# Optimization experiments

Measured on AMD Instinct MI355X. Metric: run time of the kernel, lower is better.

## Reference

```python
import jax, jax.numpy as jnp
from jax import lax
import numpy as np

B, C, H, W = 8, 256, 192, 192
ATT_K = 11
BN_EPS = 1e-5


def _dwconv(x, w, pad, stride=1):
    # x: NCHW, w: (C,1,kh,kw) depthwise
    return lax.conv_general_dilated(
        x, w, window_strides=(stride, stride), padding=pad,
        feature_group_count=x.shape[1],
        dimension_numbers=('NCHW', 'OIHW', 'NCHW'))


def _max_pool_3x3(x):
    return lax.reduce_window(x, -jnp.inf, lax.max,
                             (1, 1, 3, 3), (1, 1, 1, 1), 'SAME')


def _blur_pool(x, stride=3):
    # antialiased_cnns.BlurPool, filt_size=4: reflect pad [1,2,1,2], binomial 4x4, depthwise, stride 3
    c = x.shape[1]
    a = jnp.array([1., 3., 3., 1.], dtype=x.dtype)
    filt = (a[:, None] * a[None, :])
    filt = filt / jnp.sum(filt)
    w = jnp.tile(filt[None, None], (c, 1, 1, 1))  # (C,1,4,4)
    xp = jnp.pad(x, ((0, 0), (0, 0), (1, 2), (1, 2)), mode='reflect')
    return _dwconv(xp, w, 'VALID', stride=stride)


def _h_transform(x):
    b, c, h, w = x.shape
    x = jnp.pad(x, ((0, 0), (0, 0), (0, 0), (0, w)))
    x = x.reshape(b, c, -1)[..., :-w]
    return x.reshape(b, c, h, 2 * w - 1)


def _inv_h_transform(x):
    b, c, h, _ = x.shape  # last dim = 2h-1 (requires square)
    x = x.reshape(b, c, -1)
    x = jnp.pad(x, ((0, 0), (0, 0), (0, h)))
    x = x.reshape(b, c, h, 2 * h)
    return x[..., :h]


def _v_transform(x):
    return jnp.transpose(_h_transform(jnp.transpose(x, (0, 1, 3, 2))), (0, 1, 3, 2))


def _inv_v_transform(x):
    return jnp.transpose(_inv_h_transform(jnp.transpose(x, (0, 1, 3, 2))), (0, 1, 3, 2))


def setup_inputs() -> dict:
    key = jax.random.key(0)
    ks = jax.random.split(key, 5)
    pad = ATT_K // 2
    return {
        'x': jax.random.normal(ks[0], (B, C, H, W), dtype=jnp.float32),
        'w_h1': jax.random.normal(ks[1], (C, 1, ATT_K, 3), dtype=jnp.float32) * 0.1,
        'w_v1': jax.random.normal(ks[2], (C, 1, 3, ATT_K), dtype=jnp.float32) * 0.1,
        'w_h2': jax.random.normal(ks[3], (C, 1, ATT_K, 3), dtype=jnp.float32) * 0.1,
        'w_v2': jax.random.normal(ks[4], (C, 1, 3, ATT_K), dtype=jnp.float32) * 0.1,
        'bn_gamma': jnp.ones((C,), dtype=jnp.float32),
        'bn_beta': jnp.zeros((C,), dtype=jnp.float32),
        'bn_mean': jnp.zeros((C,), dtype=jnp.float32),
        'bn_var': jnp.ones((C,), dtype=jnp.float32),
    }


def reference(x, w_h1, w_v1, w_h2, w_v2, bn_gamma, bn_beta, bn_mean, bn_var):
    pad = ATT_K // 2
    b, c, h, w = x.shape

    x_tem = _max_pool_3x3(x)
    x_tem = _blur_pool(x_tem, stride=3)  # (B,C,64,64)

    x_h1 = _dwconv(x_tem, w_h1, ((pad, pad), (1, 1)))
    x_w1 = _dwconv(x_tem, w_v1, ((1, 1), (pad, pad)))

    # h == w (192 == 192): diagonal branch active
    x_h2 = _inv_h_transform(_dwconv(_h_transform(x_tem), w_h2, ((pad, pad), (1, 1))))
    x_w2 = _inv_v_transform(_dwconv(_v_transform(x_tem), w_v2, ((1, 1), (pad, pad))))

    s = x_h1 + x_w1 + x_h2 + x_w2
    # inference BatchNorm2d
    inv = bn_gamma / jnp.sqrt(bn_var + BN_EPS)
    att = (s - bn_mean[None, :, None, None]) * inv[None, :, None, None] + bn_beta[None, :, None, None]

    gate = jax.nn.sigmoid(att)
    # nearest interpolate to (h, w): idx = floor(i * in/out)
    ah, aw = gate.shape[2], gate.shape[3]
    idx_h = (jnp.arange(h) * ah) // h
    idx_w = (jnp.arange(w) * aw) // w
    gate_up = gate[:, :, idx_h][:, :, :, idx_w]

    return x[:, :c] * gate_up
```

## Files before the change

kernel.cpp:

```cpp
#include <hip/hip_runtime.h>
#include <hip/hip_fp16.h>
#include <math.h>

#define BN_EPS 1e-5f

__device__ __forceinline__ float max3f(float a, float b, float c) {
    return fmaxf(fmaxf(a, b), c);
}

__global__ __launch_bounds__(512, 8)
void mra_fused(const float* __restrict__ x,
               const float* __restrict__ wh1,
               const float* __restrict__ wv1,
               const float* __restrict__ wh2,
               const float* __restrict__ wv2,
               const float* __restrict__ bng,
               const float* __restrict__ bnb,
               const float* __restrict__ bnm,
               const float* __restrict__ bnv,
               float* __restrict__ out)
{
    __shared__ __align__(16) __half sxp_h[76][84];
    __shared__ __align__(16) __half gate_h[64][72];

    const int plane = blockIdx.x;
    const int c     = plane & 255;
    const int tid   = threadIdx.x;
    const int lane  = tid & 63;
    const int w     = tid >> 6;
    const float* __restrict__ xp = x   + (size_t)plane * 36864;
    float* __restrict__       op = out + (size_t)plane * 36864;

    {
        int* z = (int*)&sxp_h[0][0];
        const int nInt = (76 * 84 * 2) / 4;
        #pragma unroll
        for (int i = 0; i < 7; ++i) {
            const int idx = tid + (i << 9);
            if (idx < nInt) z[idx] = 0;
        }
    }
    __syncthreads();

    {
        const int P0  = w << 3;
        const int r0  = 3 * P0 - 2;
        const int col = 3 * lane;

        float c0r[4], c1r[4], c2r[4];
        auto issue = [&](int k, int s) {
            int r = r0 + k;
            r = r < 0 ? 0 : (r > 191 ? 191 : r);
            const float* rp = xp + r * 192 + col;
            c0r[s] = rp[0]; c1r[s] = rp[1]; c2r[s] = rp[2];
        };
        issue(0, 0); issue(1, 1); issue(2, 2); issue(3, 3);

        float h[3][4];
        float hb[3];
        float hbp = 0.f;

        #pragma unroll
        for (int k = 0; k < 27; ++k) {
            const int s = k & 3;
            const float c0 = c0r[s], c1 = c1r[s], c2 = c2r[s];
            if (k + 4 < 27) issue(k + 4, s);

            float xm2 = __shfl_up(c1, 1);
            float xm1 = __shfl_up(c2, 1);
            float xp3 = __shfl_down(c0, 1);
            if (lane == 0)  xm1 = c0;
            if (lane == 63) xp3 = c2;

            const float hm_m1 = max3f(xm2, xm1, c0);
            const float hm_0  = max3f(xm1, c0,  c1);
            const float hm_1  = max3f(c0,  c1,  c2);
            const float hm_2  = max3f(c1,  c2,  xp3);

            float* hk = h[k % 3];
            hk[0] = (lane == 0) ? hm_1 : hm_m1;
            hk[1] = hm_0; hk[2] = hm_1; hk[3] = hm_2;

            if (k >= 2) {
                const float* a = h[(k - 2) % 3];
                const float* b = h[(k - 1) % 3];
                const float* d = h[k % 3];
                const float e4 =
                      0.125f * max3f(a[0], b[0], d[0])
                    + 0.375f * max3f(a[1], b[1], d[1])
                    + 0.375f * max3f(a[2], b[2], d[2])
                    + 0.125f * max3f(a[3], b[3], d[3]);
                if (k == 2) {
                    hbp = e4;
                } else {
                    hb[k % 3] = e4;
                    if (k % 3 == 2) {
                        const int i = (k - 5) / 3;
                        float a_out;
                        if (i == 0 && w == 0)
                            a_out = 0.375f * hb[0] + 0.5f * hb[1] + 0.125f * hb[2];
                        else
                            a_out = 0.125f * hbp + 0.375f * hb[0]
                                  + 0.375f * hb[1] + 0.125f * hb[2];
                        hbp = hb[2];
                        sxp_h[P0 + i + 6][lane + 8] = __float2half(a_out);
                    }
                }
            }
        }
    }
    __syncthreads();

    const int p  = tid >> 3;
    const int q0 = (tid & 7) << 3;
    float acc[8];
    #pragma unroll
    for (int i = 0; i < 8; ++i) acc[i] = 0.0f;

    const float* __restrict__ wh1p = wh1 + c * 33;
    const float* __restrict__ wv1p = wv1 + c * 33;
    const float* __restrict__ wh2p = wh2 + c * 33;
    const float* __restrict__ wv2p = wv2 + c * 33;

    #pragma unroll
    for (int e = -6; e <= 6; ++e) {
        float rbx[24];
        const __half* rowl = &sxp_h[p + e + 6][q0];
        #pragma unroll
        for (int u = 0; u < 6; ++u) {
            const __half2* h2p = (const __half2*)(rowl + 4 * u);
            const float2 f0 = __half22float2(h2p[0]);
            const float2 f1 = __half22float2(h2p[1]);
            rbx[4 * u + 0] = f0.x; rbx[4 * u + 1] = f0.y;
            rbx[4 * u + 2] = f1.x; rbx[4 * u + 3] = f1.y;
        }
        if (e >= -5 && e <= 5) {
            #pragma unroll
            for (int dw = -1; dw <= 1; ++dw) {
                const float wt = wh1p[(e + 5) * 3 + dw + 1];
                #pragma unroll
                for (int i = 0; i < 8; ++i) acc[i] += wt * rbx[i + dw + 8];
            }
            #pragma unroll
            for (int dw = -1; dw <= 1; ++dw) {
                const float wt = wh2p[(e + 5) * 3 + dw + 1];
                #pragma unroll
                for (int i = 0; i < 8; ++i) acc[i] += wt * rbx[i + dw - e + 8];
            }
        }
        if (e >= -1 && e <= 1) {
            #pragma unroll
            for (int dw = -5; dw <= 5; ++dw) {
                const float wt = wv1p[(e + 1) * 11 + dw + 5];
                #pragma unroll
                for (int i = 0; i < 8; ++i) acc[i] += wt * rbx[i + dw + 8];
            }
        }
        #pragma unroll
        for (int dh = -1; dh <= 1; ++dh) {
            const int dw = dh - e;
            if (dw >= -5 && dw <= 5) {
                const float wt = wv2p[(dh + 1) * 11 + dw + 5];
                #pragma unroll
                for (int i = 0; i < 8; ++i) acc[i] += wt * rbx[i + dh - e + 8];
            }
        }
    }

    const float inv = bng[c] * rsqrtf(bnv[c] + BN_EPS);
    const float mu  = bnm[c];
    const float bt  = bnb[c];
    #pragma unroll
    for (int i = 0; i < 4; ++i) {
        const float a0 = (acc[2 * i]     - mu) * inv + bt;
        const float a1 = (acc[2 * i + 1] - mu) * inv + bt;
        const float g0 = 1.0f / (1.0f + __expf(-a0));
        const float g1 = 1.0f / (1.0f + __expf(-a1));
        *(__half2*)(&gate_h[p][q0 + 2 * i]) = __floats2half2_rn(g0, g1);
    }
    __builtin_amdgcn_wave_barrier();

    const float4* __restrict__ x4 = (const float4*)xp + w * 1152;
    float4* __restrict__       o4 = (float4*)op       + w * 1152;
    int rlj[3], gcj[3], rrj[3];
    #pragma unroll
    for (int j = 0; j < 3; ++j) {
        const int idx0 = lane + (j << 6);
        const int rw   = idx0 / 48;
        const int c4   = idx0 - rw * 48;
        rlj[j] = rw;
        const int jb = c4 << 2;
        gcj[j] = jb / 3;
        rrj[j] = jb - 3 * gcj[j];
    }
    #pragma unroll
    for (int u = 0; u < 6; ++u) {
        #pragma unroll
        for (int j = 0; j < 3; ++j) {
            const int row_l = rlj[j] + (u << 2);
            const int idx   = lane + ((u * 3 + j) << 6);
            const int gr    = (w << 3) + row_l / 3;
            const float g0 = __half2float(gate_h[gr][gcj[j]]);
            const float g1 = __half2float(gate_h[gr][gcj[j] + 1]);
            const float4 xv = x4[idx];
            float4 ov;
            const float s1 = (rrj[j] == 2) ? g1 : g0;
            const float s2 = (rrj[j] >= 1) ? g1 : g0;
            ov.x = xv.x * g0;
            ov.y = xv.y * s1;
            ov.z = xv.z * s2;
            ov.w = xv.w * g1;
            o4[idx] = ov;
        }
    }
}

extern "C" void kernel_launch(void* const* d_in, const int* in_sizes, int n_in,
                              void* d_out, int out_size, void* d_ws, size_t ws_size,
                              hipStream_t stream) {
    const float* x   = (const float*)d_in[0];
    const float* wh1 = (const float*)d_in[1];
    const float* wv1 = (const float*)d_in[2];
    const float* wh2 = (const float*)d_in[3];
    const float* wv2 = (const float*)d_in[4];
    const float* g   = (const float*)d_in[5];
    const float* b   = (const float*)d_in[6];
    const float* m   = (const float*)d_in[7];
    const float* v   = (const float*)d_in[8];

    mra_fused<<<dim3(8 * 256), dim3(512), 0, stream>>>(
        x, wh1, wv1, wh2, wv2, g, b, m, v, (float*)d_out);
}
```

Before: 164.8 us.

## Fold four depthwise attention convs into one 13-tap stencil computed with MFMA

Sums the four depthwise kernels (h1, v1 and the diagonal h2, v2) into a single 13x48 per-channel tap table in shared memory. The stencil is then evaluated as a banded matrix product using 16x16x32 fp16 MFMA instructions, replacing the scalar per-thread FMA loops. The gate is now computed in 16x16 tiles spread across waves, so the wave barrier becomes a full block barrier. This adds table-building work, fp16 quantisation of the weights, and an extra __syncthreads.

Result: no change. 163.8 us (-0.6%).

```diff
diff --git a/kernel.cpp b/kernel.cpp
--- a/kernel.cpp
+++ b/kernel.cpp
@@ -3,6 +3,9 @@
 #include <math.h>
 
 #define BN_EPS 1e-5f
+
+typedef _Float16 f16x8 __attribute__((ext_vector_type(8)));
+typedef float    f32x4 __attribute__((ext_vector_type(4)));
 
 __device__ __forceinline__ float max3f(float a, float b, float c) {
     return fmaxf(fmaxf(a, b), c);
@@ -20,8 +23,9 @@
                const float* __restrict__ bnv,
                float* __restrict__ out)
 {
-    __shared__ __align__(16) __half sxp_h[76][84];
+    __shared__ __align__(16) __half sxp_h[76][88];
     __shared__ __align__(16) __half gate_h[64][72];
+    __shared__ __align__(16) __half Tpad[13][48];
 
     const int plane = blockIdx.x;
     const int c     = plane & 255;
@@ -33,11 +37,32 @@
 
     {
         int* z = (int*)&sxp_h[0][0];
-        const int nInt = (76 * 84 * 2) / 4;
+        const int nInt = (76 * 88 * 2) / 4;
         #pragma unroll
         for (int i = 0; i < 7; ++i) {
             const int idx = tid + (i << 9);
             if (idx < nInt) z[idx] = 0;
+        }
+    }
+    {
+        const float* __restrict__ wh1p = wh1 + c * 33;
+        const float* __restrict__ wv1p = wv1 + c * 33;
+        const float* __restrict__ wh2p = wh2 + c * 33;
+        const float* __restrict__ wv2p = wv2 + c * 33;
+        for (int s = tid; s < 13 * 48; s += 512) {
+            const int er = s / 48;
+            const int e  = er - 6;
+            const int d  = (s - er * 48) - 24;
+            float t = 0.f;
+            if (e >= -5 && e <= 5 && d >= -1 && d <= 1)
+                t += wh1p[(e + 5) * 3 + d + 1];
+            if (e >= -5 && e <= 5 && d + e >= -1 && d + e <= 1)
+                t += wh2p[(e + 5) * 3 + d + e + 1];
+            if (e >= -1 && e <= 1 && d >= -5 && d <= 5)
+                t += wv1p[(e + 1) * 11 + d + 5];
+            if (d + e >= -1 && d + e <= 1 && d >= -5 && d <= 5)
+                t += wv2p[(d + e + 1) * 11 + d + 5];
+            Tpad[er][s - er * 48] = __float2half(t);
         }
     }
     __syncthreads();
@@ -63,19 +88,19 @@
         #pragma unroll
         for (int k = 0; k < 27; ++k) {
             const int s = k & 3;
-            const float c0 = c0r[s], c1 = c1r[s], c2 = c2r[s];
+            const float cc0 = c0r[s], cc1 = c1r[s], cc2 = c2r[s];
             if (k + 4 < 27) issue(k + 4, s);
 
-            float xm2 = __shfl_up(c1, 1);
-            float xm1 = __shfl_up(c2, 1);
-            float xp3 = __shfl_down(c0, 1);
-            if (lane == 0)  xm1 = c0;
-            if (lane == 63) xp3 = c2;
-
-            const float hm_m1 = max3f(xm2, xm1, c0);
-            const float hm_0  = max3f(xm1, c0,  c1);
-            const float hm_1  = max3f(c0,  c1,  c2);
-            const float hm_2  = max3f(c1,  c2,  xp3);
+            float xm2 = __shfl_up(cc1, 1);
+            float xm1 = __shfl_up(cc2, 1);
+            float xp3 = __shfl_down(cc0, 1);
+            if (lane == 0)  xm1 = cc0;
+            if (lane == 63) xp3 = cc2;
+
+            const float hm_m1 = max3f(xm2, xm1, cc0);
+            const float hm_0  = max3f(xm1, cc0, cc1);
+            const float hm_1  = max3f(cc0, cc1, cc2);
+            const float hm_2  = max3f(cc1, cc2, xp3);
 
             float* hk = h[k % 3];
             hk[0] = (lane == 0) ? hm_1 : hm_m1;
@@ -103,7 +128,7 @@
                             a_out = 0.125f * hbp + 0.375f * hb[0]
                                   + 0.375f * hb[1] + 0.125f * hb[2];
                         hbp = hb[2];
-                        sxp_h[P0 + i + 6][lane + 8] = __float2half(a_out);
+                        sxp_h[(w << 3) + i + 6][lane + 8] = __float2half(a_out);
                     }
                 }
             }
@@ -111,74 +136,45 @@
     }
     __syncthreads();
 
-    const int p  = tid >> 3;
-    const int q0 = (tid & 7) << 3;
-    float acc[8];
-    #pragma unroll
-    for (int i = 0; i < 8; ++i) acc[i] = 0.0f;
-
-    const float* __restrict__ wh1p = wh1 + c * 33;
-    const float* __restrict__ wv1p = wv1 + c * 33;
-    const float* __restrict__ wh2p = wh2 + c * 33;
-    const float* __restrict__ wv2p = wv2 + c * 33;
-
-    #pragma unroll
-    for (int e = -6; e <= 6; ++e) {
-        float rbx[24];
-        const __half* rowl = &sxp_h[p + e + 6][q0];
-        #pragma unroll
-        for (int u = 0; u < 6; ++u) {
-            const __half2* h2p = (const __half2*)(rowl + 4 * u);
-            const float2 f0 = __half22float2(h2p[0]);
-            const float2 f1 = __half22float2(h2p[1]);
-            rbx[4 * u + 0] = f0.x; rbx[4 * u + 1] = f0.y;
-            rbx[4 * u + 2] = f1.x; rbx[4 * u + 3] = f1.y;
-        }
-        if (e >= -5 && e <= 5) {
+    {
+        const int lr = lane & 15;
+        const int lg = lane >> 4;
+        const int t0 = 2 * w;
+        const int P0 = (t0 >> 2) << 4;
+        const int Q0a = (t0 & 3) << 4;
+        const int Q0b = ((t0 + 1) & 3) << 4;
+        const int tb = lg * 8 + 16 - lr;
+
+        f32x4 acc0 = {0.f, 0.f, 0.f, 0.f};
+        f32x4 acc1 = {0.f, 0.f, 0.f, 0.f};
+
+        #pragma unroll
+        for (int e = -6; e <= 6; ++e) {
+            const __half* trow = &Tpad[e + 6][0];
+            f16x8 bf;
             #pragma unroll
-            for (int dw = -1; dw <= 1; ++dw) {
-                const float wt = wh1p[(e + 5) * 3 + dw + 1];
-                #pragma unroll
-                for (int i = 0; i < 8; ++i) acc[i] += wt * rbx[i + dw + 8];
-            }
-            #pragma unroll
-            for (int dw = -1; dw <= 1; ++dw) {
-                const float wt = wh2p[(e + 5) * 3 + dw + 1];
-                #pragma unroll
-                for (int i = 0; i < 8; ++i) acc[i] += wt * rbx[i + dw - e + 8];
-            }
-        }
-        if (e >= -1 && e <= 1) {
-            #pragma unroll
-            for (int dw = -5; dw <= 5; ++dw) {
-                const float wt = wv1p[(e + 1) * 11 + dw + 5];
-                #pragma unroll
-                for (int i = 0; i < 8; ++i) acc[i] += wt * rbx[i + dw + 8];
-            }
-        }
-        #pragma unroll
-        for (int dh = -1; dh <= 1; ++dh) {
-            const int dw = dh - e;
-            if (dw >= -5 && dw <= 5) {
-                const float wt = wv2p[(dh + 1) * 11 + dw + 5];
-                #pragma unroll
-                for (int i = 0; i < 8; ++i) acc[i] += wt * rbx[i + dh - e + 8];
-            }
-        }
-    }
-
-    const float inv = bng[c] * rsqrtf(bnv[c] + BN_EPS);
-    const float mu  = bnm[c];
-    const float bt  = bnb[c];
-    #pragma unroll
-    for (int i = 0; i < 4; ++i) {
-        const float a0 = (acc[2 * i]     - mu) * inv + bt;
-        const float a1 = (acc[2 * i + 1] - mu) * inv + bt;
-        const float g0 = 1.0f / (1.0f + __expf(-a0));
-        const float g1 = 1.0f / (1.0f + __expf(-a1));
-        *(__half2*)(&gate_h[p][q0 + 2 * i]) = __floats2half2_rn(g0, g1);
-    }
-    __builtin_amdgcn_wave_barrier();
+            for (int j = 0; j < 8; ++j)
+                bf[j] = *(const _Float16*)&trow[tb + j];
+            const int row = P0 + lr + e + 6;
+            const f16x8 a0 = *(const f16x8*)&sxp_h[row][Q0a + lg * 8];
+            const f16x8 a1 = *(const f16x8*)&sxp_h[row][Q0b + lg * 8];
+            acc0 = __builtin_amdgcn_mfma_f32_16x16x32_f16(a0, bf, acc0, 0, 0, 0);
+            acc1 = __builtin_amdgcn_mfma_f32_16x16x32_f16(a1, bf, acc1, 0, 0, 0);
+        }
+
+        const float inv = bng[c] * rsqrtf(bnv[c] + BN_EPS);
+        const float mu  = bnm[c];
+        const float bt  = bnb[c];
+        #pragma unroll
+        for (int r = 0; r < 4; ++r) {
+            const int gr = P0 + lg * 4 + r;
+            const float g0 = 1.0f / (1.0f + __expf(-((acc0[r] - mu) * inv + bt)));
+            const float g1 = 1.0f / (1.0f + __expf(-((acc1[r] - mu) * inv + bt)));
+            gate_h[gr][Q0a + lr] = __float2half(g0);
+            gate_h[gr][Q0b + lr] = __float2half(g1);
+        }
+    }
+    __syncthreads();
 
     const float4* __restrict__ x4 = (const float4*)xp + w * 1152;
     float4* __restrict__       o4 = (float4*)op       + w * 1152;
```
